# Performance work log

Measured on AMD Instinct MI355X. Metric: run time of the kernel, lower is better.

The kernel has to match this reference:

```python
import jax, jax.numpy as jnp
import numpy as np
import math

IN_DIM = 2048
OUT_DIM = 14951
BATCH = 4096
EPS = 1e-12  # keras/tf l2_normalize epsilon


def _hadamard(n):
    # Sylvester construction, n must be a power of 2
    H = np.array([[1]], dtype=np.int8)
    while H.shape[0] < n:
        H = np.block([[H, H], [H, -H]]).astype(np.int8)
    return H


def setup_inputs() -> dict:
    key = jax.random.key(0)
    kx, kb = jax.random.split(key)
    x = jax.random.normal(kx, (BATCH, IN_DIM), dtype=jnp.float32)
    hsize = 2 ** int(math.ceil(math.log2(max(IN_DIM, OUT_DIM))))  # 16384
    hadamard = jnp.asarray(_hadamard(hsize)[:IN_DIM, :OUT_DIM], dtype=jnp.float32)
    init_scale = 1.0 / math.sqrt(OUT_DIM)
    scale = jnp.full((1,), init_scale, dtype=jnp.float32)
    bias = jax.random.uniform(kb, (OUT_DIM,), minval=-init_scale, maxval=init_scale, dtype=jnp.float32)
    return {"x": x, "hadamard": hadamard, "scale": scale, "bias": bias}


def reference(x, hadamard, scale, bias):
    # l2-normalize along features (tf.nn.l2_normalize semantics)
    norm = jnp.sqrt(jnp.maximum(jnp.sum(x * x, axis=-1, keepdims=True), EPS))
    xn = x / norm
    # [B, IN] @ [IN, OUT] -> [B, OUT]; scale is a learned scalar, negated
    out = -scale * jnp.matmul(xn, hadamard)
    out = out + bias
    # activation=None in this config
    return out
```

## Files before the change

### kernel.cpp

```cpp
#include <hip/hip_runtime.h>


#define IN_DIM 2048
#define OUT_DIM 14951
#define BATCH 4096

__global__ __launch_bounds__(256) void HadamardClassifier_74586402062910_kernel(
    const float* __restrict__ x,
    const float* __restrict__ scale,
    const float* __restrict__ bias,
    float* __restrict__ out)
{
    const int lane = threadIdx.x & 63;
    const int wave = threadIdx.x >> 6;
    const int row  = blockIdx.x * 4 + wave;

    const float* __restrict__ xr = x + (size_t)row * IN_DIM;

    float v[32];
    float ss = 0.f;
    #pragma unroll
    for (int r = 0; r < 32; ++r) {
        float t = xr[r * 64 + lane];
        v[r] = t;
        ss = fmaf(t, t, ss);
    }

    #pragma unroll
    for (int s = 1; s < 64; s <<= 1)
        ss += __shfl_xor(ss, s, 64);

    const float norm   = sqrtf(fmaxf(ss, 1e-12f));
    const float factor = -scale[0] / norm;

    #pragma unroll
    for (int s = 1; s < 64; s <<= 1) {
        const bool hi = (lane & s) != 0;
        #pragma unroll
        for (int r = 0; r < 32; ++r) {
            float t = __shfl_xor(v[r], s, 64);
            v[r] = hi ? (t - v[r]) : (v[r] + t);
        }
    }

    #pragma unroll
    for (int sr = 1; sr < 32; sr <<= 1) {
        #pragma unroll
        for (int r = 0; r < 32; ++r) {
            if ((r & sr) == 0) {
                const float a = v[r], b = v[r | sr];
                v[r]      = a + b;
                v[r | sr] = a - b;
            }
        }
    }

    #pragma unroll
    for (int r = 0; r < 32; ++r) v[r] *= factor;

    float* __restrict__ orow = out + (size_t)row * OUT_DIM;

    for (int g = 0; g < 7; ++g) {
        const int mbase = g * 32;
        #pragma unroll
        for (int mm = 0; mm < 32; ++mm) {
            const int j = (mbase + mm) * 64 + lane;
            orow[j] = v[mm] + bias[j];
        }
    }
    #pragma unroll
    for (int mm = 0; mm < 9; ++mm) {
        const int j = (224 + mm) * 64 + lane;
        orow[j] = v[mm] + bias[j];
    }
    if (lane < 39) {
        const int j = 233 * 64 + lane;
        orow[j] = v[9] + bias[j];
    }
}

extern "C" void kernel_launch(void* const* d_in, const int* in_sizes, int n_in,
                              void* d_out, int out_size, void* d_ws, size_t ws_size,
                              hipStream_t stream) {
    const float* x     = (const float*)d_in[0];
    const float* scale = (const float*)d_in[2];
    const float* bias  = (const float*)d_in[3];
    float* out = (float*)d_out;

    dim3 grid(BATCH / 4);
    dim3 block(256);
    HadamardClassifier_74586402062910_kernel<<<grid, block, 0, stream>>>(x, scale, bias, out);
}
```

Before: 335.1 us.

## Vectorize Hadamard row loads and output stores with float4 and nontemporal writes

Each lane now loads 4 contiguous x elements with 128-bit loads, and the element-to-lane mapping is rearranged so the butterfly stages work on the new layout: an intra-lane radix-4 first stage, the 64-lane shuffle stages, then the remaining register stages. Output rows are written as 4-wide nontemporal stores, with bias read as float4. The goal is fewer memory instructions on this write-bound kernel and less cache pollution from the large output. The risk is that OUT_DIM is odd, so output rows are not 16-byte aligned. The stores therefore use an unaligned vector type, which may be split by the hardware, and a scalar tail handles the last three elements.

```diff
diff --git a/kernel.cpp b/kernel.cpp
--- a/kernel.cpp
+++ b/kernel.cpp
@@ -4,6 +4,9 @@
 #define IN_DIM 2048
 #define OUT_DIM 14951
 #define BATCH 4096
+
+typedef float f32x4  __attribute__((ext_vector_type(4)));
+typedef float f32x4u __attribute__((ext_vector_type(4), aligned(4)));
 
 __global__ __launch_bounds__(256) void HadamardClassifier_74586402062910_kernel(
     const float* __restrict__ x,
@@ -15,67 +18,96 @@
     const int wave = threadIdx.x >> 6;
     const int row  = blockIdx.x * 4 + wave;
 
-    const float* __restrict__ xr = x + (size_t)row * IN_DIM;
+    const f32x4* __restrict__ x4 =
+        reinterpret_cast<const f32x4*>(x + (size_t)row * IN_DIM);
 
     float v[32];
     float ss = 0.f;
     #pragma unroll
-    for (int r = 0; r < 32; ++r) {
-        float t = xr[r * 64 + lane];
-        v[r] = t;
-        ss = fmaf(t, t, ss);
+    for (int r = 0; r < 8; ++r) {
+        f32x4 t = x4[r * 64 + lane];
+        #pragma unroll
+        for (int k = 0; k < 4; ++k) {
+            v[4*r + k] = t[k];
+            ss = fmaf(t[k], t[k], ss);
+        }
     }
 
     #pragma unroll
-    for (int s = 1; s < 64; s <<= 1)
-        ss += __shfl_xor(ss, s, 64);
+    for (int s = 1; s < 64; s <<= 1) ss += __shfl_xor(ss, s, 64);
+    const float factor = -scale[0] / sqrtf(fmaxf(ss, 1e-12f));
 
-    const float norm   = sqrtf(fmaxf(ss, 1e-12f));
-    const float factor = -scale[0] / norm;
+    #pragma unroll
+    for (int r = 0; r < 8; ++r) {
+        const float a0 = v[4*r+0], a1 = v[4*r+1], a2 = v[4*r+2], a3 = v[4*r+3];
+        const float s01 = a0 + a1, d01 = a0 - a1, s23 = a2 + a3, d23 = a2 - a3;
+        v[4*r+0] = s01 + s23;  v[4*r+1] = d01 + d23;
+        v[4*r+2] = s01 - s23;  v[4*r+3] = d01 - d23;
+    }
 
     #pragma unroll
     for (int s = 1; s < 64; s <<= 1) {
         const bool hi = (lane & s) != 0;
         #pragma unroll
-        for (int r = 0; r < 32; ++r) {
-            float t = __shfl_xor(v[r], s, 64);
-            v[r] = hi ? (t - v[r]) : (v[r] + t);
+        for (int i = 0; i < 32; ++i) {
+            const float t = __shfl_xor(v[i], s, 64);
+            v[i] = hi ? (t - v[i]) : (v[i] + t);
         }
     }
 
     #pragma unroll
-    for (int sr = 1; sr < 32; sr <<= 1) {
+    for (int sr = 1; sr < 8; sr <<= 1) {
         #pragma unroll
-        for (int r = 0; r < 32; ++r) {
+        for (int r = 0; r < 8; ++r) {
             if ((r & sr) == 0) {
-                const float a = v[r], b = v[r | sr];
-                v[r]      = a + b;
-                v[r | sr] = a - b;
+                #pragma unroll
+                for (int k = 0; k < 4; ++k) {
+                    const float a = v[4*r + k], b = v[4*(r|sr) + k];
+                    v[4*r + k]      = a + b;
+                    v[4*(r|sr) + k] = a - b;
+                }
             }
         }
     }
 
     #pragma unroll
-    for (int r = 0; r < 32; ++r) v[r] *= factor;
+    for (int i = 0; i < 32; ++i) v[i] *= factor;
 
     float* __restrict__ orow = out + (size_t)row * OUT_DIM;
+    const int l4 = lane * 4;
 
     for (int g = 0; g < 7; ++g) {
-        const int mbase = g * 32;
+        const int base = g * 2048 + l4;
         #pragma unroll
-        for (int mm = 0; mm < 32; ++mm) {
-            const int j = (mbase + mm) * 64 + lane;
-            orow[j] = v[mm] + bias[j];
+        for (int m = 0; m < 8; ++m) {
+            const int off = base + m * 256;
+            const f32x4 b4 = *reinterpret_cast<const f32x4*>(bias + off);
+            f32x4u o;
+            o[0] = v[4*m+0] + b4[0];  o[1] = v[4*m+1] + b4[1];
+            o[2] = v[4*m+2] + b4[2];  o[3] = v[4*m+3] + b4[3];
+            __builtin_nontemporal_store(o, reinterpret_cast<f32x4u*>(orow + off));
         }
     }
     #pragma unroll
-    for (int mm = 0; mm < 9; ++mm) {
-        const int j = (224 + mm) * 64 + lane;
-        orow[j] = v[mm] + bias[j];
+    for (int m = 0; m < 2; ++m) {
+        const int off = (56 + m) * 256 + l4;
+        const f32x4 b4 = *reinterpret_cast<const f32x4*>(bias + off);
+        f32x4u o;
+        o[0] = v[4*m+0] + b4[0];  o[1] = v[4*m+1] + b4[1];
+        o[2] = v[4*m+2] + b4[2];  o[3] = v[4*m+3] + b4[3];
+        __builtin_nontemporal_store(o, reinterpret_cast<f32x4u*>(orow + off));
     }
-    if (lane < 39) {
-        const int j = 233 * 64 + lane;
-        orow[j] = v[9] + bias[j];
+    if (lane < 25) {
+        const int off = 14848 + l4;
+        const f32x4 b4 = *reinterpret_cast<const f32x4*>(bias + off);
+        f32x4u o;
+        o[0] = v[8]  + b4[0];  o[1] = v[9]  + b4[1];
+        o[2] = v[10] + b4[2];  o[3] = v[11] + b4[3];
+        __builtin_nontemporal_store(o, reinterpret_cast<f32x4u*>(orow + off));
+    } else if (lane == 25) {
+        orow[14948] = v[8]  + bias[14948];
+        orow[14949] = v[9]  + bias[14949];
+        orow[14950] = v[10] + bias[14950];
     }
 }
 
```

New measurement: 343.6 us. 2.5% more time.
